# Kernel tuning notes

Measured on AMD Instinct MI355X. Metric: run time of the kernel, lower is better.

Reference implementation:

```python
import jax, jax.numpy as jnp
import numpy as np

N, F, C, H, E, G, L = 50000, 128, 64, 4, 500000, 32, 4
EPS = 1e-5
NEG_SLOPE = 0.2


def setup_inputs() -> dict:
    key = jax.random.key(0)
    ks = jax.random.split(key, 16)
    x = jax.random.normal(ks[0], (N, F), dtype=jnp.float32)
    edge_index = jax.random.randint(ks[1], (2, E), 0, N, dtype=jnp.int64)
    batch = jnp.sort(jax.random.randint(ks[2], (N,), 0, G, dtype=jnp.int64))
    s = 0.05
    params = {
        'Wp': jax.random.normal(ks[3], (F, C), jnp.float32) * s,          # initial_proj (no bias)
        'Wl': jax.random.normal(ks[4], (L, C, H * C), jnp.float32) * s,   # GATv2 lin_l per layer
        'bl': jax.random.normal(ks[5], (L, H * C), jnp.float32) * s,
        'Wr': jax.random.normal(ks[6], (L, C, H * C), jnp.float32) * s,   # GATv2 lin_r per layer
        'br': jax.random.normal(ks[7], (L, H * C), jnp.float32) * s,
        'att': jax.random.normal(ks[8], (L, H, C), jnp.float32) * s,      # attention vector per head
        'cb': jax.random.normal(ks[9], (L, C), jnp.float32) * s,          # conv output bias (concat=False)
        'ln_w': jnp.ones((L, C), jnp.float32),                            # pyg LayerNorm affine
        'ln_b': jnp.zeros((L, C), jnp.float32),
        'Wh': jax.random.normal(ks[10], (C, 1), jnp.float32) * s,         # head
        'bh': jnp.zeros((1,), jnp.float32),
    }
    return {'x': x, 'edge_index': edge_index, 'batch': batch, **params}


def _gatv2(x, src, dst, Wl, bl, Wr, br, att, cb):
    # x: [N, C] -> per-head projections [N, H, C]
    xl = (x @ Wl + bl).reshape(N, H, C)
    xr = (x @ Wr + br).reshape(N, H, C)
    # edge-wise GATv2 scores: leaky_relu(x_i + x_j) . att   -> [E, H]
    e = jax.nn.leaky_relu(xl[src] + xr[dst], NEG_SLOPE)
    score = jnp.einsum('ehc,hc->eh', e, att)
    # segment softmax over incoming edges of each destination node
    m = jax.ops.segment_max(score, dst, num_segments=N)[dst]
    p = jnp.exp(score - m)
    denom = jax.ops.segment_sum(p, dst, num_segments=N)[dst]
    alpha = p / denom                                     # [E, H]
    msg = xl[src] * alpha[..., None]                      # [E, H, C]
    out = jax.ops.segment_sum(msg, dst, num_segments=N)   # [N, H, C]
    return out.mean(axis=1) + cb                          # concat=False: head mean + bias


def _graph_norm(x, w, b):
    # pyg.nn.LayerNorm mode='graph' with batch=None: normalize over ALL elements
    xc = x - x.mean()
    std = jnp.sqrt(xc.var())
    return (xc / (std + EPS)) * w + b


def reference(x, edge_index, batch, Wp, Wl, bl, Wr, br, att, cb, ln_w, ln_b, Wh, bh):
    src, dst = edge_index[0], edge_index[1]
    h = x @ Wp
    for l in range(L):
        h = _gatv2(h, src, dst, Wl[l], bl[l], Wr[l], br[l], att[l], cb[l])
        h = jax.nn.selu(_graph_norm(h, ln_w[l], ln_b[l]))
    # global mean pool over graphs
    counts = jax.ops.segment_sum(jnp.ones((N,), h.dtype), batch, num_segments=G)
    pooled = jax.ops.segment_sum(h, batch, num_segments=G) / jnp.maximum(counts, 1.0)[:, None]
    return (pooled @ Wh + bh).squeeze(-1)  # [G]
```

## Files before the change

### kernel.cpp

```cpp
#include <hip/hip_runtime.h>
#include <hip/hip_bf16.h>
#include <hip/hip_fp8.h>
#include <math.h>

#define NN 50000
#define FIN 128
#define CC 64
#define HH 4
#define HC 256
#define EE 500000
#define GG 32
#define LL 4

typedef __hip_bfloat16 bf16;
typedef __attribute__((ext_vector_type(2))) float f2;
typedef __attribute__((ext_vector_type(8))) short s8v;
typedef __attribute__((ext_vector_type(4))) float f4v;

__device__ __forceinline__ float b2f(bf16 v){ return __bfloat162float(v); }
__device__ __forceinline__ bf16 f2b(float v){ return __float2bfloat16(v); }
__device__ __forceinline__ void unpack2(unsigned u, float& a, float& b){
  union { unsigned q; float f; } x, y;
  x.q = u << 16; y.q = u & 0xffff0000u; a = x.f; b = y.f;
}
__device__ __forceinline__ f2 unpackf2(unsigned u){
  union { unsigned q; float f; } x, y;
  x.q = u << 16; y.q = u & 0xffff0000u;
  f2 r; r.x = x.f; r.y = y.f; return r;
}
__device__ __forceinline__ f2 maxf2(f2 a, f2 b){
#if __has_builtin(__builtin_elementwise_max)
  return __builtin_elementwise_max(a, b);
#else
  f2 r; r.x = fmaxf(a.x, b.x); r.y = fmaxf(a.y, b.y); return r;
#endif
}
__device__ __forceinline__ float clamp4(float v){ return fminf(fmaxf(v, -1e4f), 1e4f); }
__device__ __forceinline__ unsigned pack2bf(float a, float b){
  bf16 x = f2b(clamp4(a)), y = f2b(clamp4(b));
  unsigned short ux = *(unsigned short*)&x, uy = *(unsigned short*)&y;
  return (unsigned)ux | ((unsigned)uy << 16);
}
__device__ __forceinline__ unsigned f4_to_fp8x4(float a, float b, float c, float d){
  a = fminf(fmaxf(a, -240.f), 240.f);
  b = fminf(fmaxf(b, -240.f), 240.f);
  c = fminf(fmaxf(c, -240.f), 240.f);
  d = fminf(fmaxf(d, -240.f), 240.f);
#if __has_builtin(__builtin_amdgcn_cvt_pk_fp8_f32)
  int p = 0;
  p = __builtin_amdgcn_cvt_pk_fp8_f32(a, b, p, false);
  p = __builtin_amdgcn_cvt_pk_fp8_f32(c, d, p, true);
  return (unsigned)p;
#else
  __hip_fp8_e4m3 qa(a), qb(b), qc(c), qd(d);
  return (unsigned)qa.__x | ((unsigned)qb.__x << 8) | ((unsigned)qc.__x << 16) | ((unsigned)qd.__x << 24);
#endif
}
__device__ __forceinline__ void fp8x4_to_f2(unsigned u, f2& lo, f2& hi){
#if __has_builtin(__builtin_amdgcn_cvt_pk_f32_fp8)
  lo = __builtin_amdgcn_cvt_pk_f32_fp8((int)u, false);
  hi = __builtin_amdgcn_cvt_pk_f32_fp8((int)u, true);
#else
  __hip_fp8_e4m3 q0, q1, q2, q3;
  q0.__x = u & 0xff; q1.__x = (u >> 8) & 0xff; q2.__x = (u >> 16) & 0xff; q3.__x = (u >> 24) & 0xff;
  lo.x = (float)q0; lo.y = (float)q1; hi.x = (float)q2; hi.y = (float)q3;
#endif
}
__device__ __forceinline__ float selu_f(float y){
  const float SS = 1.0507009873554805f, SA = 1.6732632423543772f;
  return y > 0.f ? SS*y : SS*SA*(__expf(y) - 1.f);
}
__device__ __forceinline__ f2 shxor_f2(f2 v, int m){
  f2 r; r.x = __shfl_xor(v.x, m, 64); r.y = __shfl_xor(v.y, m, 64); return r;
}
__device__ __forceinline__ int ld_i(const void* p, int i, int w8){
  if (w8) return (int)((const long long*)p)[i];
  return ((const int*)p)[i];
}
__device__ __forceinline__ void stats_inline(const float* __restrict__ partials, float& mu, float& inv){
  float s1 = 0.f, s2 = 0.f;
  #pragma unroll 8
  for (int i = 0; i < 64; ++i){ s1 += partials[i]; s2 += partials[64 + i]; }
  float cnt = (float)NN * 64.f;
  mu = s1 / cnt;
  float var = s2 / cnt - mu*mu;
  if (!(var > 0.f)) var = 0.f;
  inv = 1.0f / (sqrtf(var) + 1e-5f);
}

__global__ __launch_bounds__(256) void k_setup(
    const void* ei, const void* batch,
    const void* Wp, const void* Wl, const void* bl, const void* Wr, const void* br,
    const void* att, const void* cb, const void* lnw, const void* lnb,
    const void* Wh, const void* bh,
    float* dst, int* deg, float* pooled, int* flags, short* apack){
  int b = blockIdx.x;
  int t = threadIdx.x;
  const unsigned short* lw = (const unsigned short*)lnw;
  int f32 = (lw[0] == 0x0000 && lw[1] == 0x3F80) ? 1 : 0;
  if (b < 560){
    int i = b*256 + t;
    if (i < 143169){
      const void* src; int idx;
      if      (i < 8192)   { src = Wp;  idx = i; }
      else if (i < 73728)  { src = Wl;  idx = i - 8192; }
      else if (i < 74752)  { src = bl;  idx = i - 73728; }
      else if (i < 140288) { src = Wr;  idx = i - 74752; }
      else if (i < 141312) { src = br;  idx = i - 140288; }
      else if (i < 142336) { src = att; idx = i - 141312; }
      else if (i < 142592) { src = cb;  idx = i - 142336; }
      else if (i < 142848) { src = lnw; idx = i - 142592; }
      else if (i < 143104) { src = lnb; idx = i - 142848; }
      else if (i < 143168) { src = Wh;  idx = i - 143104; }
      else                 { src = bh;  idx = 0; }
      dst[i] = f32 ? ((const float*)src)[idx] : b2f(((const bf16*)src)[idx]);
    }
  } else if (b < 756){
    int i = (b - 560)*256 + t;
    if (i < NN) deg[i] = 0;
  } else if (b == 756){
    for (int i = t; i < GG*64; i += 256) pooled[i] = 0.f;
    if (t < 64){
      int lane = t;
      const int* w  = (const int*)ei;
      const int* wb = (const int*)batch;
      int bad_e = (lane < 32) ? (w[2*(lane*15625) + 1] != 0) : 0;
      int bad_b = (lane < 32) ? (wb[25001 + 2*lane] != 0) : 0;
      unsigned long long me = __ballot(bad_e);
      unsigned long long mb = __ballot(bad_b);
      if (lane == 0){
        flags[0] = (me == 0ULL) ? 1 : 0;
        flags[1] = (mb == 0ULL) ? 1 : 0;
        flags[2] = f32;
      }
    }
  } else {
    int i2 = (b - 757)*256 + t;
    int l   = i2 >> 15;
    int rem = i2 & 32767;
    int ct  = rem >> 10;
    int rem2 = rem & 1023;
    int kh  = rem2 >> 9;
    int li  = (rem2 >> 3) & 63;
    int j   = rem2 & 7;
    int k   = kh*32 + ((li >> 4) << 3) + j;
    int c   = (ct << 4) + (li & 15);
    const void* Wsrc = (c < 256) ? Wl : Wr;
    int cc = c & 255;
    size_t idx = ((size_t)l*64 + k)*256 + cc;
    float v = f32 ? ((const float*)Wsrc)[idx] : b2f(((const bf16*)Wsrc)[idx]);
    bf16 bv = f2b(v);
    apack[i2] = *(short*)&bv;
  }
}

__global__ __launch_bounds__(256) void k_hist(const void* __restrict__ ei, int* __restrict__ deg,
                                              const int* __restrict__ flags){
  int e = blockIdx.x*256 + threadIdx.x;
  if (e < EE){
    int d = ld_i(ei, EE + e, flags[0]);
    if ((unsigned)d < NN) atomicAdd(&deg[d], 1);
  }
}

__global__ __launch_bounds__(256) void k_scan1(const int* __restrict__ deg, int* __restrict__ off,
                                               int* __restrict__ btot){
  int t = threadIdx.x;
  int i = blockIdx.x*256 + t;
  int v = (i < NN) ? deg[i] : 0;
  int incl = v;
  #pragma unroll
  for (int dl = 1; dl < 64; dl <<= 1){
    int u = __shfl_up(incl, dl, 64);
    if ((t & 63) >= dl) incl += u;
  }
  __shared__ int wt[4];
  if ((t & 63) == 63) wt[t >> 6] = incl;
  __syncthreads();
  int base = 0;
  for (int ww = 0; ww < (t >> 6); ++ww) base += wt[ww];
  incl += base;
  if (i < NN) off[i + 1] = incl;
  if (t == 255) btot[blockIdx.x] = incl;
}

__global__ __launch_bounds__(256) void k_scan2(const int* __restrict__ btot, int* __restrict__ boff, int nb){
  int t = threadIdx.x;
  int v = (t < nb) ? btot[t] : 0;
  int incl = v;
  #pragma unroll
  for (int dl = 1; dl < 64; dl <<= 1){
    int u = __shfl_up(incl, dl, 64);
    if ((t & 63) >= dl) incl += u;
  }
  __shared__ int wt[4];
  if ((t & 63) == 63) wt[t >> 6] = incl;
  __syncthreads();
  int base = 0;
  for (int ww = 0; ww < (t >> 6); ++ww) base += wt[ww];
  incl += base;
  if (t < 256) boff[t] = incl - v;
}

__global__ __launch_bounds__(256) void k_scan3(int* __restrict__ off, int* __restrict__ cursor,
                                               const int* __restrict__ deg, const int* __restrict__ boff){
  int i = blockIdx.x*256 + threadIdx.x;
  if (i >= NN) return;
  int v = off[i + 1] + boff[i >> 8];
  off[i + 1] = v;
  cursor[i] = v - deg[i];
  if (i == 0) off[0] = 0;
}

__global__ __launch_bounds__(256) void k_scatter_gb(const void* __restrict__ ei, int* __restrict__ cursor,
                                                    int* __restrict__ ssrc, const void* __restrict__ batch,
                                                    int* __restrict__ gstart, const int* __restrict__ flags){
  int b = blockIdx.x;
  if (b < 1954){
    int e = b*256 + threadIdx.x;
    if (e < EE){
      int f = flags[0];
      int s = ld_i(ei, e, f);
      int d = ld_i(ei, EE + e, f);
      if ((unsigned)d < NN && (unsigned)s < NN){
        int p = atomicAdd(&cursor[d], 1);
        ssrc[p] = s << 8;
      }
    }
  } else {
    int i = (b - 1954)*256 + threadIdx.x;
    if (i >= NN) return;
    int f = flags[1];
    int bb = ld_i(batch, i, f);
    bb = min(max(bb, 0), GG - 1);
    if (i == 0){ for (int q = 0; q <= bb; ++q) gstart[q] = 0; }
    else {
      int pb = ld_i(batch, i - 1, f);
      pb = min(max(pb, 0), GG - 1);
      for (int q = pb + 1; q <= bb; ++q) gstart[q] = i;
    }
    if (i == NN - 1){ for (int q = bb + 1; q <= GG; ++q) gstart[q] = NN; }
  }
}

__global__ __launch_bounds__(256) void k_proj(const void* __restrict__ xraw, const float* __restrict__ Wp32,
                                              bf16* __restrict__ h, const int* __restrict__ flags){
  __shared__ float xs[64*128];
  __shared__ float wsm[128*64];
  int t = threadIdx.x;
  int r0 = blockIdx.x * 64;
  int rows = NN - r0; if (rows > 64) rows = 64;
  const float4* gw = (const float4*)Wp32;
  #pragma unroll
  for (int i = 0; i < 8; ++i) ((float4*)wsm)[i*256 + t] = gw[i*256 + t];
  int f32 = flags[2];
  #pragma unroll
  for (int i = 0; i < 8; ++i){
    int p = i*256 + t;
    int r = p >> 5, kq = p & 31;
    float4 v = make_float4(0.f,0.f,0.f,0.f);
    if (r < rows){
      if (f32) v = ((const float4*)xraw)[(size_t)(r0 + r)*32 + kq];
      else {
        uint2 u = ((const uint2*)xraw)[(size_t)(r0 + r)*32 + kq];
        unpack2(u.x, v.x, v.y); unpack2(u.y, v.z, v.w);
      }
    }
    *(float4*)&xs[r*128 + kq*4] = v;
  }
  __syncthreads();
  int tx = t & 15, ty = t >> 4;
  int c0 = tx*4, rr0 = ty*4;
  float acc[4][4] = {{0.f}};
  for (int k = 0; k < 128; k += 4){
    float4 xv[4];
    #pragma unroll
    for (int i = 0; i < 4; ++i) xv[i] = *(const float4*)&xs[(rr0 + i)*128 + k];
    const float* xf = (const float*)xv;
    #pragma unroll
    for (int m = 0; m < 4; ++m){
      float4 wv = *(const float4*)&wsm[(k + m)*64 + c0];
      #pragma unroll
      for (int i = 0; i < 4; ++i){
        float xm = xf[i*4 + m];
        acc[i][0] = fmaf(xm, wv.x, acc[i][0]);
        acc[i][1] = fmaf(xm, wv.y, acc[i][1]);
        acc[i][2] = fmaf(xm, wv.z, acc[i][2]);
        acc[i][3] = fmaf(xm, wv.w, acc[i][3]);
      }
    }
  }
  #pragma unroll
  for (int i = 0; i < 4; ++i){
    int r = rr0 + i;
    if (r < rows){
      uint2 pk;
      pk.x = pack2bf(acc[i][0], acc[i][1]);
      pk.y = pack2bf(acc[i][2], acc[i][3]);
      *(uint2*)((unsigned char*)h + (size_t)(r0 + r)*128 + c0*2) = pk;
    }
  }
}

__global__ __launch_bounds__(256) void k_gemm2m(const bf16* __restrict__ h,
    const s8v* __restrict__ apack,
    const float* __restrict__ bl, const float* __restrict__ br,
    unsigned char* __restrict__ xl8, unsigned char* __restrict__ xr8,
    const float* __restrict__ partials, const float* __restrict__ lnw, const float* __restrict__ lnb,
    int apply){
  __shared__ short buf[64*264];
  int t = threadIdx.x;
  int r0 = blockIdx.x * 64;
  int rows = NN - r0; if (rows > 64) rows = 64;
  float mu = 0.f, inv = 0.f;
  if (apply) stats_inline(partials, mu, inv);
  #pragma unroll
  for (int i = 0; i < 4; ++i){
    int p = i*256 + t;
    int r = p >> 4, kq = p & 15;
    uint2 pk; pk.x = 0u; pk.y = 0u;
    if (r < rows){
      uint2 hv = ((const uint2*)h)[(size_t)(r0 + r)*16 + kq];
      if (apply){
        float4 v;
        unpack2(hv.x, v.x, v.y); unpack2(hv.y, v.z, v.w);
        float4 w4 = *(const float4*)(lnw + kq*4);
        float4 b4 = *(const float4*)(lnb + kq*4);
        v.x = selu_f((v.x - mu)*inv*w4.x + b4.x);
        v.y = selu_f((v.y - mu)*inv*w4.y + b4.y);
        v.z = selu_f((v.z - mu)*inv*w4.z + b4.z);
        v.w = selu_f((v.w - mu)*inv*w4.w + b4.w);
        pk.x = pack2bf(v.x, v.y);
        pk.y = pack2bf(v.z, v.w);
      } else {
        pk = hv;
      }
    }
    *(uint2*)&buf[r*264 + kq*4] = pk;
  }
  __syncthreads();
  int wave = t >> 6, lane = t & 63;
  int n = lane & 15, q = lane >> 4;
  int rowb = wave * 16;
  s8v bf0 = *(const s8v*)&buf[(rowb + n)*264 + q*8];
  s8v bf1 = *(const s8v*)&buf[(rowb + n)*264 + 32 + q*8];
  __syncthreads();
  unsigned* ubuf = (unsigned*)buf;
  {
    #pragma unroll 4
    for (int cc = 0; cc < 16; ++cc){
      s8v a0 = apack[cc*128 + lane];
      s8v a1 = apack[cc*128 + 64 + lane];
      f4v acc = {0.f, 0.f, 0.f, 0.f};
      acc = __builtin_amdgcn_mfma_f32_16x16x32_bf16(a0, bf0, acc, 0, 0, 0);
      acc = __builtin_amdgcn_mfma_f32_16x16x32_bf16(a1, bf1, acc, 0, 0, 0);
      int colh = (cc << 4) + (q << 2);
      float4 bb = *(const float4*)&bl[colh];
      ubuf[(rowb + n)*132 + (colh >> 2)] =
          f4_to_fp8x4(acc[0] + bb.x, acc[1] + bb.y, acc[2] + bb.z, acc[3] + bb.w);
    }
    __syncthreads();
    #pragma unroll
    for (int i = 0; i < 16; ++i){
      int idx = i*256 + t;
      int row = idx >> 6, colu = idx & 63;
      if (row < rows){
        unsigned v = ubuf[row*132 + colu];
        ((unsigned*)xl8)[((size_t)(r0 + row))*64 + colu] = v;
      }
    }
    __syncthreads();
  }
  {
    #pragma unroll 4
    for (int cc = 0; cc < 16; ++cc){
      int ct = 16 + cc;
      s8v a0 = apack[ct*128 + lane];
      s8v a1 = apack[ct*128 + 64 + lane];
      f4v acc = {0.f, 0.f, 0.f, 0.f};
      acc = __builtin_amdgcn_mfma_f32_16x16x32_bf16(a0, bf0, acc, 0, 0, 0);
      acc = __builtin_amdgcn_mfma_f32_16x16x32_bf16(a1, bf1, acc, 0, 0, 0);
      int colh = (cc << 4) + (q << 2);
      float4 bb = *(const float4*)&br[colh];
      ubuf[(rowb + n)*132 + (colh >> 2)] =
          f4_to_fp8x4(acc[0] + bb.x, acc[1] + bb.y, acc[2] + bb.z, acc[3] + bb.w);
    }
    __syncthreads();
    #pragma unroll
    for (int i = 0; i < 16; ++i){
      int idx = i*256 + t;
      int row = idx >> 6, colu = idx & 63;
      if (row < rows){
        unsigned v = ubuf[row*132 + colu];
        ((unsigned*)xr8)[((size_t)(r0 + row))*64 + colu] = v;
      }
    }
  }
}

__global__ __launch_bounds__(256) void k_gat(const unsigned char* __restrict__ xl8,
    const unsigned char* __restrict__ xr8,
    const int* __restrict__ off, const int* __restrict__ ssrc,
    const float* __restrict__ att, const float* __restrict__ cbp,
    bf16* __restrict__ out, float2* __restrict__ nstat){
  int t = threadIdx.x;
  int wave = t >> 6, lane = t & 63;
  int d = blockIdx.x*4 + wave;
  if (d >= NN) return;
  int s0 = off[d], s1 = off[d + 1];
  int last = s1 - 1;
  int half = lane >> 5;
  int l5 = lane & 31;
  int hh = l5 >> 3;
  int ch0 = (l5 & 7) * 8;
  const float* ap = att + hh*64 + ch0;
  float4 a4 = *(const float4*)ap;
  float4 b4 = *(const float4*)(ap + 4);
  f2 av01; av01.x = a4.x; av01.y = a4.y;
  f2 av23; av23.x = a4.z; av23.y = a4.w;
  f2 av45; av45.x = b4.x; av45.y = b4.y;
  f2 av67; av67.x = b4.z; av67.y = b4.w;
  uint2 ur8 = *(const uint2*)(xr8 + (size_t)d*256 + ((unsigned)l5 << 3));
  f2 r01, r23, r45, r67;
  fp8x4_to_f2(ur8.x, r01, r23);
  fp8x4_to_f2(ur8.y, r45, r67);
  const float NS = 0.2f;

  float den = 0.f;
  f2 m01 = {0.f,0.f}, m23 = {0.f,0.f}, m45 = {0.f,0.f}, m67 = {0.f,0.f};
  if (last >= s0){
    int ee = s0 + half; ee = ee <= last ? ee : last;
    int of = ssrc[ee];
    uint2 u = *(const uint2*)(xl8 + (size_t)(unsigned)of + ((unsigned)l5 << 3));
    for (int e = s0; e <= last; e += 2){
      int en = e + 2 + half; en = en <= last ? en : last;
      int ofn = ssrc[en];
      uint2 un = *(const uint2*)(xl8 + (size_t)(unsigned)ofn + ((unsigned)l5 << 3));
      f2 x01, x23, x45, x67;
      fp8x4_to_f2(u.x, x01, x23);
      fp8x4_to_f2(u.y, x45, x67);
      f2 t01 = x01 + r01, t23 = x23 + r23, t45 = x45 + r45, t67 = x67 + r67;
      t01 = maxf2(t01, t01*NS); t23 = maxf2(t23, t23*NS);
      t45 = maxf2(t45, t45*NS); t67 = maxf2(t67, t67*NS);
      f2 s2 = av01*t01 + av23*t23 + av45*t45 + av67*t67;
      float s = s2.x + s2.y;
      s += __shfl_xor(s, 1, 64);
      s += __shfl_xor(s, 2, 64);
      s += __shfl_xor(s, 4, 64);
      float p = __expf(fminf(s, 30.f));
      p = (e + half <= last) ? p : 0.f;
      den += p;
      m01 += x01*p; m23 += x23*p; m45 += x45*p; m67 += x67*p;
      u = un;
    }
  }
  den += __shfl_xor(den, 32, 64);
  m01 = m01 + shxor_f2(m01, 32);
  m23 = m23 + shxor_f2(m23, 32);
  m45 = m45 + shxor_f2(m45, 32);
  m67 = m67 + shxor_f2(m67, 32);
  float iv = den > 0.f ? 1.0f / den : 0.f;
  f2 v01 = m01*iv, v23 = m23*iv, v45 = m45*iv, v67 = m67*iv;
  v01 = v01 + shxor_f2(v01, 8);  v23 = v23 + shxor_f2(v23, 8);
  v45 = v45 + shxor_f2(v45, 8);  v67 = v67 + shxor_f2(v67, 8);
  v01 = v01 + shxor_f2(v01, 16); v23 = v23 + shxor_f2(v23, 16);
  v45 = v45 + shxor_f2(v45, 16); v67 = v67 + shxor_f2(v67, 16);
  if (lane < 8){
    float4 cba = *(const float4*)(cbp + lane*8);
    float4 cbb = *(const float4*)(cbp + lane*8 + 4);
    float4 oA, oB;
    oA.x = clamp4(0.25f*v01.x + cba.x);
    oA.y = clamp4(0.25f*v01.y + cba.y);
    oA.z = clamp4(0.25f*v23.x + cba.z);
    oA.w = clamp4(0.25f*v23.y + cba.w);
    oB.x = clamp4(0.25f*v45.x + cbb.x);
    oB.y = clamp4(0.25f*v45.y + cbb.y);
    oB.z = clamp4(0.25f*v67.x + cbb.z);
    oB.w = clamp4(0.25f*v67.y + cbb.w);
    uint4 pk;
    pk.x = pack2bf(oA.x, oA.y); pk.y = pack2bf(oA.z, oA.w);
    pk.z = pack2bf(oB.x, oB.y); pk.w = pack2bf(oB.z, oB.w);
    *(uint4*)((unsigned char*)out + (size_t)d*128 + lane*16) = pk;
    float s1p = oA.x + oA.y + oA.z + oA.w + oB.x + oB.y + oB.z + oB.w;
    float s2p = oA.x*oA.x + oA.y*oA.y + oA.z*oA.z + oA.w*oA.w
              + oB.x*oB.x + oB.y*oB.y + oB.z*oB.z + oB.w*oB.w;
    s1p += __shfl_xor(s1p, 1, 64); s2p += __shfl_xor(s2p, 1, 64);
    s1p += __shfl_xor(s1p, 2, 64); s2p += __shfl_xor(s2p, 2, 64);
    s1p += __shfl_xor(s1p, 4, 64); s2p += __shfl_xor(s2p, 4, 64);
    if (lane == 0){
      float2 ns; ns.x = s1p; ns.y = s2p;
      nstat[d] = ns;
    }
  }
}

__global__ __launch_bounds__(256) void k_nstat(const float2* __restrict__ nstat, float* __restrict__ partials){
  int t = threadIdx.x;
  int gid = blockIdx.x*256 + t;
  float s1 = 0.f, s2 = 0.f;
  for (int i = gid; i < NN; i += 64*256){
    float2 v = nstat[i];
    s1 += v.x; s2 += v.y;
  }
  #pragma unroll
  for (int dl = 1; dl < 64; dl <<= 1){ s1 += __shfl_xor(s1, dl, 64); s2 += __shfl_xor(s2, dl, 64); }
  __shared__ float l1[4], l2[4];
  int w = t >> 6;
  if ((t & 63) == 0){ l1[w] = s1; l2[w] = s2; }
  __syncthreads();
  if (t == 0){
    partials[blockIdx.x]      = l1[0] + l1[1] + l1[2] + l1[3];
    partials[64 + blockIdx.x] = l2[0] + l2[1] + l2[2] + l2[3];
  }
}

__global__ __launch_bounds__(256) void k_poolA(const bf16* __restrict__ h, const void* __restrict__ batch,
                                               float* __restrict__ pooled, const int* __restrict__ flags,
                                               const float* __restrict__ partials,
                                               const float* __restrict__ lnw, const float* __restrict__ lnb){
  int t = threadIdx.x;
  int c = t & 63, rq = t >> 6;
  int r0 = blockIdx.x * 256;
  int r1 = r0 + 256; if (r1 > NN) r1 = NN;
  int f = flags[1];
  float mu, inv;
  stats_inline(partials, mu, inv);
  float wc = lnw[c], bc = lnb[c];
  float acc = 0.f;
  int cur_g = -1;
  for (int r = r0 + rq; r < r1; r += 4){
    int g = ld_i(batch, r, f);
    g = min(max(g, 0), GG - 1);
    if (g != cur_g){
      if (cur_g >= 0) atomicAdd(&pooled[cur_g*64 + c], acc);
      acc = 0.f; cur_g = g;
    }
    acc += selu_f((b2f(h[(size_t)r*64 + c]) - mu)*inv*wc + bc);
  }
  if (cur_g >= 0) atomicAdd(&pooled[cur_g*64 + c], acc);
}

__global__ __launch_bounds__(64) void k_poolB(const float* __restrict__ pooled, const int* __restrict__ gstart,
    const float* __restrict__ Wh, const float* __restrict__ bh, void* __restrict__ outp,
    const int* __restrict__ flags){
  int g = blockIdx.x, t = threadIdx.x;
  int rs = gstart[g], re = gstart[g + 1];
  int cnt = re - rs; if (cnt < 1) cnt = 1;
  float val = (pooled[g*64 + t] / (float)cnt) * Wh[t];
  #pragma unroll
  for (int dl = 1; dl < 64; dl <<= 1) val += __shfl_xor(val, dl, 64);
  if (t == 0){
    float res = val + bh[0];
    if (flags[2]) ((float*)outp)[g] = res;
    else          ((bf16*)outp)[g] = f2b(res);
  }
}

extern "C" void kernel_launch(void* const* d_in, const int* in_sizes, int n_in,
                              void* d_out, int out_size, void* d_ws, size_t ws_size,
                              hipStream_t stream) {
  const void* x     = d_in[0];
  const void* ei    = d_in[1];
  const void* batch = d_in[2];
  const void* Wp    = d_in[3];
  const void* Wl    = d_in[4];
  const void* bl    = d_in[5];
  const void* Wr    = d_in[6];
  const void* br    = d_in[7];
  const void* att   = d_in[8];
  const void* cb    = d_in[9];
  const void* lnw   = d_in[10];
  const void* lnb   = d_in[11];
  const void* Wh    = d_in[12];
  const void* bh    = d_in[13];

  char* w = (char*)d_ws;
  int*   flags  = (int*)w;     w += 256;
  int*   deg    = (int*)w;     w += 200192;
  int*   off    = (int*)w;     w += 200192;
  int*   cursor = (int*)w;     w += 200192;
  int*   btot   = (int*)w;     w += 1024;
  int*   boff   = (int*)w;     w += 1024;
  int*   gstart = (int*)w;     w += 256;
  float* partials = (float*)w; w += 2048;
  float* pooled = (float*)w;   w += GG*64*4;
  float* wcvt   = (float*)w;   w += 572928;
  short* apack  = (short*)w;   w += 262144;
  float2* nstat = (float2*)w;  w += (size_t)NN*8;
  int*   ssrc   = (int*)w;     w += (size_t)EE*4;
  bf16*  hbuf   = (bf16*)w;    w += (size_t)NN*128;
  unsigned char* xlb = (unsigned char*)w; w += (size_t)NN*256;
  unsigned char* xrb = (unsigned char*)w; w += (size_t)NN*256;

  float* Wp32  = wcvt;
  float* bl32  = wcvt + 73728;
  float* br32  = wcvt + 140288;
  float* att32 = wcvt + 141312;
  float* cb32  = wcvt + 142336;
  float* lnw32 = wcvt + 142592;
  float* lnb32 = wcvt + 142848;
  float* Wh32  = wcvt + 143104;
  float* bh32  = wcvt + 143168;

  const int NB = (NN + 255) / 256;
  const int NT = (NN + 63) / 64;

  k_setup<<<757 + 512, 256, 0, stream>>>(ei, batch, Wp, Wl, bl, Wr, br, att, cb, lnw, lnb, Wh, bh,
                                         wcvt, deg, pooled, flags, apack);
  k_hist<<<(EE + 255)/256, 256, 0, stream>>>(ei, deg, flags);
  k_scan1<<<NB, 256, 0, stream>>>(deg, off, btot);
  k_scan2<<<1, 256, 0, stream>>>(btot, boff, NB);
  k_scan3<<<NB, 256, 0, stream>>>(off, cursor, deg, boff);
  k_scatter_gb<<<1954 + NB, 256, 0, stream>>>(ei, cursor, ssrc, batch, gstart, flags);

  k_proj<<<NT, 256, 0, stream>>>(x, Wp32, hbuf, flags);

  for (int l = 0; l < LL; ++l){
    int lp = (l > 0) ? (l - 1) : 0;
    k_gemm2m<<<NT, 256, 0, stream>>>(hbuf,
        (const s8v*)(apack + (size_t)l*32768),
        bl32 + (size_t)l*256, br32 + (size_t)l*256, xlb, xrb,
        partials, lnw32 + (size_t)lp*CC, lnb32 + (size_t)lp*CC, l > 0 ? 1 : 0);
    k_gat<<<(NN + 3)/4, 256, 0, stream>>>(xlb, xrb, off, ssrc,
        att32 + (size_t)l*HH*CC, cb32 + (size_t)l*CC, hbuf, nstat);
    k_nstat<<<64, 256, 0, stream>>>(nstat, partials);
  }

  k_poolA<<<NB, 256, 0, stream>>>(hbuf, batch, pooled, flags, partials,
      lnw32 + (size_t)3*CC, lnb32 + (size_t)3*CC);
  k_poolB<<<GG, 64, 0, stream>>>(pooled, gstart, Wh32, bh32, d_out, flags);
}
```

Before: 502.7 us.

## Fuse norm-stat reduction into GAT kernel and merge small launches

Removes the per-layer k_nstat kernel by having each GAT block accumulate its sum and sum-of-squares into 4096 atomic slots, which the next GEMM and the pooling kernel then reduce per wave. It also merges scan2 into scan3 by recomputing each block offset with a reduction, and merges poolA and poolB using a last-block ticket. Together this cuts about six kernel launches and the nstat buffer traffic, at the cost of float atomics, which make the sums order-nondeterministic, and a 4096-entry reduction in every GEMM block. The early return for d>=NN was also dropped in k_gat, but the grid divides N exactly.

```diff
diff --git a/kernel.cpp b/kernel.cpp
--- a/kernel.cpp
+++ b/kernel.cpp
@@ -77,10 +77,13 @@
   if (w8) return (int)((const long long*)p)[i];
   return ((const int*)p)[i];
 }
-__device__ __forceinline__ void stats_inline(const float* __restrict__ partials, float& mu, float& inv){
+__device__ __forceinline__ void stats_pstat(const float* __restrict__ pst, int t, float& mu, float& inv){
+  int lane = t & 63;
   float s1 = 0.f, s2 = 0.f;
   #pragma unroll 8
-  for (int i = 0; i < 64; ++i){ s1 += partials[i]; s2 += partials[64 + i]; }
+  for (int i = lane; i < 4096; i += 64){ s1 += pst[i]; s2 += pst[4096 + i]; }
+  #pragma unroll
+  for (int dl = 1; dl < 64; dl <<= 1){ s1 += __shfl_xor(s1, dl, 64); s2 += __shfl_xor(s2, dl, 64); }
   float cnt = (float)NN * 64.f;
   mu = s1 / cnt;
   float var = s2 / cnt - mu*mu;
@@ -93,7 +96,7 @@
     const void* Wp, const void* Wl, const void* bl, const void* Wr, const void* br,
     const void* att, const void* cb, const void* lnw, const void* lnb,
     const void* Wh, const void* bh,
-    float* dst, int* deg, float* pooled, int* flags, short* apack){
+    float* dst, int* deg, float* pooled, int* flags, short* apack, float* pstat){
   int b = blockIdx.x;
   int t = threadIdx.x;
   const unsigned short* lw = (const unsigned short*)lnw;
@@ -120,6 +123,7 @@
     if (i < NN) deg[i] = 0;
   } else if (b == 756){
     for (int i = t; i < GG*64; i += 256) pooled[i] = 0.f;
+    if (t == 64) flags[8] = 0;
     if (t < 64){
       int lane = t;
       const int* w  = (const int*)ei;
@@ -134,7 +138,7 @@
         flags[2] = f32;
       }
     }
-  } else {
+  } else if (b < 1269){
     int i2 = (b - 757)*256 + t;
     int l   = i2 >> 15;
     int rem = i2 & 32767;
@@ -151,6 +155,9 @@
     float v = f32 ? ((const float*)Wsrc)[idx] : b2f(((const bf16*)Wsrc)[idx]);
     bf16 bv = f2b(v);
     apack[i2] = *(short*)&bv;
+  } else {
+    int i = (b - 1269)*256 + t;
+    if (i < 4*8192) pstat[i] = 0.f;
   }
 }
 
@@ -184,31 +191,22 @@
   if (t == 255) btot[blockIdx.x] = incl;
 }
 
-__global__ __launch_bounds__(256) void k_scan2(const int* __restrict__ btot, int* __restrict__ boff, int nb){
+__global__ __launch_bounds__(256) void k_scan3(int* __restrict__ off, int* __restrict__ cursor,
+                                               const int* __restrict__ deg, const int* __restrict__ btot,
+                                               int nb){
   int t = threadIdx.x;
-  int v = (t < nb) ? btot[t] : 0;
-  int incl = v;
+  int v = (t < nb && t < (int)blockIdx.x) ? btot[t] : 0;
   #pragma unroll
-  for (int dl = 1; dl < 64; dl <<= 1){
-    int u = __shfl_up(incl, dl, 64);
-    if ((t & 63) >= dl) incl += u;
-  }
-  __shared__ int wt[4];
-  if ((t & 63) == 63) wt[t >> 6] = incl;
+  for (int dl = 1; dl < 64; dl <<= 1) v += __shfl_xor(v, dl, 64);
+  __shared__ int ws[4];
+  if ((t & 63) == 0) ws[t >> 6] = v;
   __syncthreads();
-  int base = 0;
-  for (int ww = 0; ww < (t >> 6); ++ww) base += wt[ww];
-  incl += base;
-  if (t < 256) boff[t] = incl - v;
-}
-
-__global__ __launch_bounds__(256) void k_scan3(int* __restrict__ off, int* __restrict__ cursor,
-                                               const int* __restrict__ deg, const int* __restrict__ boff){
-  int i = blockIdx.x*256 + threadIdx.x;
+  int boff = ws[0] + ws[1] + ws[2] + ws[3];
+  int i = blockIdx.x*256 + t;
   if (i >= NN) return;
-  int v = off[i + 1] + boff[i >> 8];
-  off[i + 1] = v;
-  cursor[i] = v - deg[i];
+  int val = off[i + 1] + boff;
+  off[i + 1] = val;
+  cursor[i] = val - deg[i];
   if (i == 0) off[0] = 0;
 }
 
@@ -306,14 +304,14 @@
     const s8v* __restrict__ apack,
     const float* __restrict__ bl, const float* __restrict__ br,
     unsigned char* __restrict__ xl8, unsigned char* __restrict__ xr8,
-    const float* __restrict__ partials, const float* __restrict__ lnw, const float* __restrict__ lnb,
+    const float* __restrict__ pst, const float* __restrict__ lnw, const float* __restrict__ lnb,
     int apply){
   __shared__ short buf[64*264];
   int t = threadIdx.x;
   int r0 = blockIdx.x * 64;
   int rows = NN - r0; if (rows > 64) rows = 64;
   float mu = 0.f, inv = 0.f;
-  if (apply) stats_inline(partials, mu, inv);
+  if (apply) stats_pstat(pst, t, mu, inv);
   #pragma unroll
   for (int i = 0; i < 4; ++i){
     int p = i*256 + t;
@@ -402,11 +400,11 @@
     const unsigned char* __restrict__ xr8,
     const int* __restrict__ off, const int* __restrict__ ssrc,
     const float* __restrict__ att, const float* __restrict__ cbp,
-    bf16* __restrict__ out, float2* __restrict__ nstat){
+    bf16* __restrict__ out, float* __restrict__ pstat){
+  __shared__ float bs1[4], bs2[4];
   int t = threadIdx.x;
   int wave = t >> 6, lane = t & 63;
   int d = blockIdx.x*4 + wave;
-  if (d >= NN) return;
   int s0 = off[d], s1 = off[d + 1];
   int last = s1 - 1;
   int half = lane >> 5;
@@ -487,44 +485,32 @@
     s1p += __shfl_xor(s1p, 1, 64); s2p += __shfl_xor(s2p, 1, 64);
     s1p += __shfl_xor(s1p, 2, 64); s2p += __shfl_xor(s2p, 2, 64);
     s1p += __shfl_xor(s1p, 4, 64); s2p += __shfl_xor(s2p, 4, 64);
-    if (lane == 0){
-      float2 ns; ns.x = s1p; ns.y = s2p;
-      nstat[d] = ns;
-    }
-  }
-}
-
-__global__ __launch_bounds__(256) void k_nstat(const float2* __restrict__ nstat, float* __restrict__ partials){
-  int t = threadIdx.x;
-  int gid = blockIdx.x*256 + t;
-  float s1 = 0.f, s2 = 0.f;
-  for (int i = gid; i < NN; i += 64*256){
-    float2 v = nstat[i];
-    s1 += v.x; s2 += v.y;
-  }
-  #pragma unroll
-  for (int dl = 1; dl < 64; dl <<= 1){ s1 += __shfl_xor(s1, dl, 64); s2 += __shfl_xor(s2, dl, 64); }
-  __shared__ float l1[4], l2[4];
-  int w = t >> 6;
-  if ((t & 63) == 0){ l1[w] = s1; l2[w] = s2; }
+    if (lane == 0){ bs1[wave] = s1p; bs2[wave] = s2p; }
+  }
   __syncthreads();
   if (t == 0){
-    partials[blockIdx.x]      = l1[0] + l1[1] + l1[2] + l1[3];
-    partials[64 + blockIdx.x] = l2[0] + l2[1] + l2[2] + l2[3];
-  }
-}
-
-__global__ __launch_bounds__(256) void k_poolA(const bf16* __restrict__ h, const void* __restrict__ batch,
-                                               float* __restrict__ pooled, const int* __restrict__ flags,
-                                               const float* __restrict__ partials,
-                                               const float* __restrict__ lnw, const float* __restrict__ lnb){
+    float a = bs1[0] + bs1[1] + bs1[2] + bs1[3];
+    float b = bs2[0] + bs2[1] + bs2[2] + bs2[3];
+    int slot = blockIdx.x & 4095;
+    atomicAdd(&pstat[slot], a);
+    atomicAdd(&pstat[4096 + slot], b);
+  }
+}
+
+__global__ __launch_bounds__(256) void k_poolAB(const bf16* __restrict__ h, const void* __restrict__ batch,
+                                                float* __restrict__ pooled, const int* __restrict__ flags,
+                                                const float* __restrict__ pst,
+                                                const float* __restrict__ lnw, const float* __restrict__ lnb,
+                                                const int* __restrict__ gstart, const float* __restrict__ Wh,
+                                                const float* __restrict__ bh, void* __restrict__ outp,
+                                                int* __restrict__ ticket){
   int t = threadIdx.x;
   int c = t & 63, rq = t >> 6;
   int r0 = blockIdx.x * 256;
   int r1 = r0 + 256; if (r1 > NN) r1 = NN;
   int f = flags[1];
   float mu, inv;
-  stats_inline(partials, mu, inv);
+  stats_pstat(pst, t, mu, inv);
   float wc = lnw[c], bc = lnb[c];
   float acc = 0.f;
   int cur_g = -1;
@@ -538,21 +524,28 @@
     acc += selu_f((b2f(h[(size_t)r*64 + c]) - mu)*inv*wc + bc);
   }
   if (cur_g >= 0) atomicAdd(&pooled[cur_g*64 + c], acc);
-}
-
-__global__ __launch_bounds__(64) void k_poolB(const float* __restrict__ pooled, const int* __restrict__ gstart,
-    const float* __restrict__ Wh, const float* __restrict__ bh, void* __restrict__ outp,
-    const int* __restrict__ flags){
-  int g = blockIdx.x, t = threadIdx.x;
-  int rs = gstart[g], re = gstart[g + 1];
-  int cnt = re - rs; if (cnt < 1) cnt = 1;
-  float val = (pooled[g*64 + t] / (float)cnt) * Wh[t];
-  #pragma unroll
-  for (int dl = 1; dl < 64; dl <<= 1) val += __shfl_xor(val, dl, 64);
+  __threadfence();
+  __shared__ int amLast;
   if (t == 0){
-    float res = val + bh[0];
-    if (flags[2]) ((float*)outp)[g] = res;
-    else          ((bf16*)outp)[g] = f2b(res);
+    int prev = atomicAdd(ticket, 1);
+    amLast = (prev == (int)gridDim.x - 1) ? 1 : 0;
+  }
+  __syncthreads();
+  if (amLast){
+    __threadfence();
+    int lane = t & 63, w = t >> 6;
+    for (int g = w; g < GG; g += 4){
+      int rs = gstart[g], re = gstart[g + 1];
+      int cnt = re - rs; if (cnt < 1) cnt = 1;
+      float val = (pooled[g*64 + lane] / (float)cnt) * Wh[lane];
+      #pragma unroll
+      for (int dl = 1; dl < 64; dl <<= 1) val += __shfl_xor(val, dl, 64);
+      if (lane == 0){
+        float res = val + bh[0];
+        if (flags[2]) ((float*)outp)[g] = res;
+        else          ((bf16*)outp)[g] = f2b(res);
+      }
+    }
   }
 }
 
@@ -582,15 +575,15 @@
   int*   btot   = (int*)w;     w += 1024;
   int*   boff   = (int*)w;     w += 1024;
   int*   gstart = (int*)w;     w += 256;
-  float* partials = (float*)w; w += 2048;
+  float* pstat  = (float*)w;   w += 4*8192*4;
   float* pooled = (float*)w;   w += GG*64*4;
   float* wcvt   = (float*)w;   w += 572928;
   short* apack  = (short*)w;   w += 262144;
-  float2* nstat = (float2*)w;  w += (size_t)NN*8;
   int*   ssrc   = (int*)w;     w += (size_t)EE*4;
   bf16*  hbuf   = (bf16*)w;    w += (size_t)NN*128;
   unsigned char* xlb = (unsigned char*)w; w += (size_t)NN*256;
   unsigned char* xrb = (unsigned char*)w; w += (size_t)NN*256;
+  (void)boff;
 
   float* Wp32  = wcvt;
   float* bl32  = wcvt + 73728;
@@ -605,12 +598,11 @@
   const int NB = (NN + 255) / 256;
   const int NT = (NN + 63) / 64;
 
-  k_setup<<<757 + 512, 256, 0, stream>>>(ei, batch, Wp, Wl, bl, Wr, br, att, cb, lnw, lnb, Wh, bh,
-                                         wcvt, deg, pooled, flags, apack);
+  k_setup<<<757 + 512 + 128, 256, 0, stream>>>(ei, batch, Wp, Wl, bl, Wr, br, att, cb, lnw, lnb, Wh, bh,
+                                               wcvt, deg, pooled, flags, apack, pstat);
   k_hist<<<(EE + 255)/256, 256, 0, stream>>>(ei, deg, flags);
   k_scan1<<<NB, 256, 0, stream>>>(deg, off, btot);
-  k_scan2<<<1, 256, 0, stream>>>(btot, boff, NB);
-  k_scan3<<<NB, 256, 0, stream>>>(off, cursor, deg, boff);
+  k_scan3<<<NB, 256, 0, stream>>>(off, cursor, deg, btot, NB);
   k_scatter_gb<<<1954 + NB, 256, 0, stream>>>(ei, cursor, ssrc, batch, gstart, flags);
 
   k_proj<<<NT, 256, 0, stream>>>(x, Wp32, hbuf, flags);
@@ -620,13 +612,11 @@
     k_gemm2m<<<NT, 256, 0, stream>>>(hbuf,
         (const s8v*)(apack + (size_t)l*32768),
         bl32 + (size_t)l*256, br32 + (size_t)l*256, xlb, xrb,
-        partials, lnw32 + (size_t)lp*CC, lnb32 + (size_t)lp*CC, l > 0 ? 1 : 0);
+        pstat + (size_t)lp*8192, lnw32 + (size_t)lp*CC, lnb32 + (size_t)lp*CC, l > 0 ? 1 : 0);
     k_gat<<<(NN + 3)/4, 256, 0, stream>>>(xlb, xrb, off, ssrc,
-        att32 + (size_t)l*HH*CC, cb32 + (size_t)l*CC, hbuf, nstat);
-    k_nstat<<<64, 256, 0, stream>>>(nstat, partials);
-  }
-
-  k_poolA<<<NB, 256, 0, stream>>>(hbuf, batch, pooled, flags, partials,
-      lnw32 + (size_t)3*CC, lnb32 + (size_t)3*CC);
-  k_poolB<<<GG, 64, 0, stream>>>(pooled, gstart, Wh32, bh32, d_out, flags);
-}
+        att32 + (size_t)l*HH*CC, cb32 + (size_t)l*CC, hbuf, pstat + (size_t)l*8192);
+  }
+
+  k_poolAB<<<NB, 256, 0, stream>>>(hbuf, batch, pooled, flags, pstat + (size_t)3*8192,
+      lnw32 + (size_t)3*CC, lnb32 + (size_t)3*CC, gstart, Wh32, bh32, d_out, flags + 8);
+}
```

After: 523.8 us. 4.2% more time.
